# Kernel optimization log

Hardware: AMD Instinct MI355X
Metric: run time of the kernel (lower is better)

Reference implementation:

```python
import jax, jax.numpy as jnp
import numpy as np
from functools import partial

NODES = 50
IN_SZ = 12
HID = 6


def _conv(x, W, b):
    # x: [N, C, H, W], W: [O, I, 3, 3], pad 1 -> same H, W
    y = jax.lax.conv_general_dilated(x, W, window_strides=(1, 1),
                                     padding=((1, 1), (1, 1)),
                                     dimension_numbers=('NCHW', 'OIHW', 'NCHW'))
    return y + b[None, :, None, None]


def setup_inputs() -> dict:
    key = jax.random.key(0)
    ks = jax.random.split(key, 12)
    B, T = 4096, 12
    d = {}
    d['A_hat'] = jax.random.normal(ks[0], (NODES, NODES), dtype=jnp.float32)
    d['X'] = jax.random.normal(ks[1], (B, NODES, T, IN_SZ, 1), dtype=jnp.float32)
    s_ih = 1.0 / np.sqrt(HID)
    d['W_ih'] = jax.random.uniform(ks[2], (4 * HID, IN_SZ), jnp.float32, -s_ih, s_ih)
    d['W_hh'] = jax.random.uniform(ks[3], (4 * HID, HID), jnp.float32, -s_ih, s_ih)
    d['b_ih'] = jax.random.uniform(ks[4], (4 * HID,), jnp.float32, -s_ih, s_ih)
    d['b_hh'] = jax.random.uniform(ks[5], (4 * HID,), jnp.float32, -s_ih, s_ih)
    d['Wf1'] = jax.random.normal(ks[6], (100, 50, 3, 3), jnp.float32) * 0.05
    d['bf1'] = jnp.zeros((100,), jnp.float32)
    d['Wf2'] = jax.random.normal(ks[7], (100, 100, 3, 3), jnp.float32) * 0.05
    d['bf2'] = jnp.zeros((100,), jnp.float32)
    d['Wf3'] = jax.random.normal(ks[8], (50, 100, 3, 3), jnp.float32) * 0.05
    d['bf3'] = jnp.zeros((50,), jnp.float32)
    d['W_lean'] = jax.random.normal(ks[9], (HID, HID), jnp.float32) * 0.3
    d['b_lean'] = jnp.zeros((HID,), jnp.float32)
    return d


def reference(A_hat, X, W_ih, W_hh, b_ih, b_hh, Wf1, bf1, Wf2, bf2, Wf3, bf3, W_lean, b_lean):
    # out1: [S, 50, 12] with S = B*T; the Python loop over S becomes a scan
    out1 = jnp.squeeze(X, axis=4).reshape(-1, NODES, IN_SZ)

    def step(carry, x_t):
        h, c = carry  # each [50, 6]
        gates = x_t @ W_ih.T + b_ih + h @ W_hh.T + b_hh  # [50, 24]
        i, f, g, o = jnp.split(gates, 4, axis=-1)
        i = jax.nn.sigmoid(i)
        f = jax.nn.sigmoid(f)
        g = jnp.tanh(g)
        o = jax.nn.sigmoid(o)
        c_new = f * c + i * g
        h_new = o * jnp.tanh(c_new)
        h_new = jnp.tanh(h_new)  # module applies extra tanh and feeds it back
        return (h_new, c_new), h_new

    h0 = jnp.zeros((NODES, HID), dtype=X.dtype)
    c0 = jnp.zeros((NODES, HID), dtype=X.dtype)
    _, al = jax.lax.scan(step, (h0, c0), out1)  # al: [S, 50, 6]

    out2 = al.reshape(-1, NODES, HID, 1)  # [S, 50, 6, 1]
    f = jax.nn.relu(_conv(out2, Wf1, bf1))
    f = jax.nn.relu(_conv(f, Wf2, bf2))
    f = jax.nn.relu(_conv(f, Wf3, bf3))
    out = (f.reshape(-1, HID) @ W_lean.T + b_lean).reshape(-1, NODES, HID, 1)
    return out
```

## Files before the change

kernel.cpp:

```cpp
#include <hip/hip_runtime.h>

#define NCH 1536
#define CL 32
#define WM 16

typedef _Float16 half8 __attribute__((ext_vector_type(8)));
typedef float f32x4 __attribute__((ext_vector_type(4)));

#define ROWB 256
#define BUFB 17408
#define ALH_OFF 131072

__device__ __forceinline__ int swz(int srow, int b){ return srow*ROWB + (b ^ ((srow&7)<<4)); }

__device__ __forceinline__ unsigned short f2h_bits(float x){
  _Float16 h = (_Float16)x;
  return __builtin_bit_cast(unsigned short, h);
}

__device__ __forceinline__ float rcp_(float x){ return __builtin_amdgcn_rcpf(x); }
__device__ __forceinline__ float tanh_(float z){ return 1.f - 2.f*rcp_(1.f + __expf(2.f*z)); }

__global__ void pack_frags(const float* __restrict__ W1, const float* __restrict__ W2,
                           const float* __restrict__ W3, unsigned short* __restrict__ ws)
{
  int tid = blockIdx.x*256 + threadIdx.x;
  if (tid >= 174*512) return;
  int f = tid >> 9, e = tid & 511, l = e >> 3, j = e & 7;
  int d, ks, nt, I, O; const float* W;
  if (f < 42)      { int x = f;     int st = x/7;  nt = x%7; d = st/2; ks = st%2; I = 50;  O = 100; W = W1; }
  else if (f < 126){ int x = f-42;  int st = x/7;  nt = x%7; d = st/4; ks = st%4; I = 100; O = 100; W = W2; }
  else             { int x = f-126; int st = x/4;  nt = x%4; d = st/4; ks = st%4; I = 100; O = 50;  W = W3; }
  int k = ks*32 + ((l>>4)<<3) + j;
  int o = nt*16 + (l&15);
  float v = (k < I && o < O) ? W[((o*I + k)*3 + d)*3 + 1] : 0.f;
  ws[tid] = f2h_bits(v);
}

template<bool F16>
__global__ __launch_bounds__(128,2) void lstm_scan3(
    const float* __restrict__ X, const float* __restrict__ Wih,
    const float* __restrict__ Whh, const float* __restrict__ bih,
    const float* __restrict__ bhh, float* __restrict__ al32,
    unsigned short* __restrict__ al16)
{
  const int l = threadIdx.x & 63;
  const int wv = threadIdx.x >> 6;
  const int blk = blockIdx.x;
  const int p6 = blk/5, w = blk - p6*5;
  const int q = l/6, j = l - q*6;
  const bool active = (q < 10);
  const int n = w*10 + (active ? q : 0);
  const int sbase = active ? q*6 : 0;

  const int c0 = p6*6 + 3*wv;
  const int sAb = c0*CL, sBb = sAb + CL, sCb = sBb + CL;
  const int sALast = sAb + CL - 1, sBLast = sBb + CL - 1, sCLast = sCb + CL - 1;

  float wi[4][12], wh[4][6], bb[4];
  #pragma unroll
  for (int g=0; g<4; ++g){
    const int r = g*6 + j;
    const float4 w0 = *(const float4*)(Wih + r*12);
    const float4 w1 = *(const float4*)(Wih + r*12 + 4);
    const float4 w2 = *(const float4*)(Wih + r*12 + 8);
    wi[g][0]=w0.x; wi[g][1]=w0.y; wi[g][2]=w0.z; wi[g][3]=w0.w;
    wi[g][4]=w1.x; wi[g][5]=w1.y; wi[g][6]=w1.z; wi[g][7]=w1.w;
    wi[g][8]=w2.x; wi[g][9]=w2.y; wi[g][10]=w2.z; wi[g][11]=w2.w;
    const float2 h0 = *(const float2*)(Whh + r*6);
    const float2 h1 = *(const float2*)(Whh + r*6 + 2);
    const float2 h2 = *(const float2*)(Whh + r*6 + 4);
    wh[g][0]=h0.x; wh[g][1]=h0.y; wh[g][2]=h1.x;
    wh[g][3]=h1.y; wh[g][4]=h2.x; wh[g][5]=h2.y;
    bb[g] = bih[r] + bhh[r];
  }

  float hA[6], hB[6], hC[6], cA = 0.f, cB = 0.f, cC = 0.f;
  #pragma unroll
  for (int k=0;k<6;++k){ hA[k]=0.f; hB[k]=0.f; hC[k]=0.f; }

  const int sA0 = (c0==0) ? 0 : (sAb - WM);
  const int sB0 = sBb - WM;
  const int sC0 = sCb - WM;
  float4 xA0,xA1,xA2, xB0,xB1,xB2, xC0,xC1,xC2;
  { const float4* p = (const float4*)(X + (size_t)sA0*600 + n*12); xA0=p[0]; xA1=p[1]; xA2=p[2]; }
  { const float4* p = (const float4*)(X + (size_t)sB0*600 + n*12); xB0=p[0]; xB1=p[1]; xB2=p[2]; }
  { const float4* p = (const float4*)(X + (size_t)sC0*600 + n*12); xC0=p[0]; xC1=p[1]; xC2=p[2]; }

  auto step = [&](const float4& x0, const float4& x1, const float4& x2,
                  float* h, float& c) -> float {
    const float xr[12] = {x0.x,x0.y,x0.z,x0.w, x1.x,x1.y,x1.z,x1.w, x2.x,x2.y,x2.z,x2.w};
    float a0=bb[0], a1=bb[1], a2=bb[2], a3=bb[3];
    #pragma unroll
    for (int k=0;k<12;++k){ a0+=wi[0][k]*xr[k]; a1+=wi[1][k]*xr[k];
                            a2+=wi[2][k]*xr[k]; a3+=wi[3][k]*xr[k]; }
    #pragma unroll
    for (int k=0;k<6;++k){ a0+=wh[0][k]*h[k]; a1+=wh[1][k]*h[k];
                           a2+=wh[2][k]*h[k]; a3+=wh[3][k]*h[k]; }
    const float gi = rcp_(1.f + __expf(-a0));
    const float gf = rcp_(1.f + __expf(-a1));
    const float gg = 2.f*rcp_(1.f + __expf(-(a2+a2))) - 1.f;
    const float go = rcp_(1.f + __expf(-a3));
    c = gf*c + gi*gg;
    return tanh_(go * tanh_(c));
  };

  for (int i = -WM; i < CL; ++i){
    const int sA = sAb + i, sB = sBb + i, sC = sCb + i;
    const bool doA = (sA >= 0);

    float hnA = 0.f;
    if (doA){
      hnA = step(xA0,xA1,xA2, hA, cA);
      const int sn = (sA < sALast) ? sA+1 : sALast;
      const float4* xq = (const float4*)(X + (size_t)sn*600 + n*12);
      xA0 = xq[0]; xA1 = xq[1]; xA2 = xq[2];
    }
    float hnB;
    {
      hnB = step(xB0,xB1,xB2, hB, cB);
      const int sn = (sB < sBLast) ? sB+1 : sBLast;
      const float4* xq = (const float4*)(X + (size_t)sn*600 + n*12);
      xB0 = xq[0]; xB1 = xq[1]; xB2 = xq[2];
    }
    float hnC;
    {
      hnC = step(xC0,xC1,xC2, hC, cC);
      const int sn = (sC < sCLast) ? sC+1 : sCLast;
      const float4* xq = (const float4*)(X + (size_t)sn*600 + n*12);
      xC0 = xq[0]; xC1 = xq[1]; xC2 = xq[2];
    }

    if (active && i >= 0){
      const size_t oA = (size_t)sA*300 + n*6 + j;
      const size_t oB = (size_t)sB*300 + n*6 + j;
      const size_t oC = (size_t)sC*300 + n*6 + j;
      if (F16){ al16[oA] = f2h_bits(hnA); al16[oB] = f2h_bits(hnB); al16[oC] = f2h_bits(hnC); }
      else    { al32[oA] = hnA;           al32[oB] = hnB;           al32[oC] = hnC; }
    }
    #pragma unroll
    for (int k=0;k<6;++k){
      hA[k] = __shfl(hnA, sbase + k, 64);
      hB[k] = __shfl(hnB, sbase + k, 64);
      hC[k] = __shfl(hnC, sbase + k, 64);
    }
  }
}

template<int KS, int NTT, int NTG, bool LAST>
__device__ __forceinline__ void conv_layer2(
    char* lds, int inOff, int outOff, const unsigned short* __restrict__ wsU,
    int fbase, int ntOff, const float* __restrict__ bias, int O, int m0, int lane)
{
  f32x4 acc[2][NTG];
  #pragma unroll
  for (int m=0;m<2;m++)
    #pragma unroll
    for (int n=0;n<NTG;n++) acc[m][n] = (f32x4){0.f,0.f,0.f,0.f};

  const int ar = m0 + (lane & 15);
  const int abyte_g = (lane>>4)<<4;
  const int laneb = lane << 3;

  half8 a0c = *(const half8*)(lds + inOff + swz(ar, abyte_g));
  half8 a1c = *(const half8*)(lds + inOff + swz(ar + 16, abyte_g));
  half8 bc[NTG];
  {
    const unsigned short* p0 = wsU + (size_t)(fbase + ntOff)*512 + laneb;
    #pragma unroll
    for (int n=0;n<NTG;n++) bc[n] = *(const half8*)(p0 + n*512);
  }

  #pragma unroll
  for (int st=0; st<3*KS; ++st){
    half8 a0n, a1n, bn[NTG];
    if (st+1 < 3*KS){
      const int dn = (st+1)/KS, ksn = (st+1)%KS;
      a0n = *(const half8*)(lds + inOff + swz(ar + dn, ksn*64 + abyte_g));
      a1n = *(const half8*)(lds + inOff + swz(ar + 16 + dn, ksn*64 + abyte_g));
      const unsigned short* pn = wsU + (size_t)(fbase + (st+1)*NTT + ntOff)*512 + laneb;
      #pragma unroll
      for (int n=0;n<NTG;n++) bn[n] = *(const half8*)(pn + n*512);
    }
    #pragma unroll
    for (int n=0;n<NTG;n++){
      acc[0][n] = __builtin_amdgcn_mfma_f32_16x16x32_f16(a0c, bc[n], acc[0][n], 0, 0, 0);
      acc[1][n] = __builtin_amdgcn_mfma_f32_16x16x32_f16(a1c, bc[n], acc[1][n], 0, 0, 0);
    }
    if (st+1 < 3*KS){
      a0c = a0n; a1c = a1n;
      #pragma unroll
      for (int n=0;n<NTG;n++) bc[n] = bn[n];
    }
  }

  const int colBase = lane & 15;
  #pragma unroll
  for (int m=0;m<2;m++){
    const int rbase = m0 + m*16 + ((lane>>4)<<2);
    #pragma unroll
    for (int n=0;n<NTG;n++){
      const int col = (ntOff + n)*16 + colBase;
      if (col < O){
        const float b = bias[col];
        #pragma unroll
        for (int r=0;r<4;r++){
          const int crow = rbase + r;
          const int p8 = crow & 7;
          if (p8 >= 1 && p8 <= 6){
            const float v = fmaxf(acc[m][n][r] + b, 0.f);
            const int srow = crow + 1;
            if (LAST) *(float*)(lds + outOff + swz(srow, col*4)) = v;
            else      *(unsigned short*)(lds + outOff + swz(srow, col*2)) = f2h_bits(v);
          }
        }
      }
    }
  }
}

template<int KS, int NTT, int NTG>
__device__ __forceinline__ void conv_layer3_fused(
    char* lds, int inOff, const unsigned short* __restrict__ wsU,
    int fbase, int ntOff, const float* __restrict__ b3,
    const float* __restrict__ Wl, const float* __restrict__ bl,
    float* __restrict__ io, size_t base, int m0, int lane)
{
  f32x4 acc[2][NTG];
  #pragma unroll
  for (int m=0;m<2;m++)
    #pragma unroll
    for (int n=0;n<NTG;n++) acc[m][n] = (f32x4){0.f,0.f,0.f,0.f};

  const int ar = m0 + (lane & 15);
  const int abyte_g = (lane>>4)<<4;
  const int laneb = lane << 3;

  half8 a0c = *(const half8*)(lds + inOff + swz(ar, abyte_g));
  half8 a1c = *(const half8*)(lds + inOff + swz(ar + 16, abyte_g));
  half8 bc[NTG];
  {
    const unsigned short* p0 = wsU + (size_t)(fbase + ntOff)*512 + laneb;
    #pragma unroll
    for (int n=0;n<NTG;n++) bc[n] = *(const half8*)(p0 + n*512);
  }

  #pragma unroll
  for (int st=0; st<3*KS; ++st){
    half8 a0n, a1n, bn[NTG];
    if (st+1 < 3*KS){
      const int dn = (st+1)/KS, ksn = (st+1)%KS;
      a0n = *(const half8*)(lds + inOff + swz(ar + dn, ksn*64 + abyte_g));
      a1n = *(const half8*)(lds + inOff + swz(ar + 16 + dn, ksn*64 + abyte_g));
      const unsigned short* pn = wsU + (size_t)(fbase + (st+1)*NTT + ntOff)*512 + laneb;
      #pragma unroll
      for (int n=0;n<NTG;n++) bn[n] = *(const half8*)(pn + n*512);
    }
    #pragma unroll
    for (int n=0;n<NTG;n++){
      acc[0][n] = __builtin_amdgcn_mfma_f32_16x16x32_f16(a0c, bc[n], acc[0][n], 0, 0, 0);
      acc[1][n] = __builtin_amdgcn_mfma_f32_16x16x32_f16(a1c, bc[n], acc[1][n], 0, 0, 0);
    }
    if (st+1 < 3*KS){
      a0c = a0n; a1c = a1n;
      #pragma unroll
      for (int n=0;n<NTG;n++) bc[n] = bn[n];
    }
  }

  const int colBase = lane & 15;
  const int qg = lane >> 4;
  const bool hiHalf = (qg & 1);
  #pragma unroll
  for (int m=0;m<2;m++){
    const int sIdx = (m0 + m*16 + qg*4) >> 3;
    #pragma unroll
    for (int n=0;n<NTG;n++){
      const int col = (ntOff + n)*16 + colBase;
      const bool valid = (col < 50);
      const float b = valid ? b3[col] : 0.f;
      float vv[4];
      #pragma unroll
      for (int r=0;r<4;r++) vv[r] = fmaxf(acc[m][n][r] + b, 0.f);
      float tot[6];
      #pragma unroll
      for (int j=0;j<6;j++){
        float pj;
        if (!hiHalf) pj = Wl[j*6+0]*vv[1] + Wl[j*6+1]*vv[2] + Wl[j*6+2]*vv[3];
        else         pj = Wl[j*6+3]*vv[0] + Wl[j*6+4]*vv[1] + Wl[j*6+5]*vv[2];
        tot[j] = pj + __shfl_xor(pj, 16, 64);
      }
      if (valid && !hiHalf){
        float* dst = io + base + (size_t)sIdx*300 + col*6;
        float2 p0 = {tot[0]+bl[0], tot[1]+bl[1]};
        float2 p1 = {tot[2]+bl[2], tot[3]+bl[3]};
        float2 p2 = {tot[4]+bl[4], tot[5]+bl[5]};
        *(float2*)(dst+0) = p0;
        *(float2*)(dst+2) = p1;
        *(float2*)(dst+4) = p2;
      }
    }
  }
}

template<bool ALH>
__global__ __launch_bounds__(256,4) void conv_mfma_kernel(
    float* __restrict__ io, const unsigned short* __restrict__ alh,
    const unsigned short* __restrict__ wsU,
    const float* __restrict__ b1, const float* __restrict__ b2, const float* __restrict__ b3,
    const float* __restrict__ Wl, const float* __restrict__ bl)
{
  __shared__ __align__(16) char lds[2*BUFB];
  const int t = threadIdx.x;
  const int lane = t & 63, w = t >> 6;
  const int mg = w >> 1, ng = w & 1;
  const int m0 = mg*32;
  const size_t base = (size_t)blockIdx.x * 2400;

  for (int i = t; i < (2*BUFB)/16; i += 256) ((f32x4*)lds)[i] = (f32x4){0.f,0.f,0.f,0.f};
  __syncthreads();

  if (ALH){
    const unsigned short* ap = alh + base;
    for (int idx = t; idx < 400; idx += 256){
      const int s = idx/50, n = idx - (idx/50)*50;
      const unsigned short* pp = ap + s*300 + n*6;
      const int r0 = s*8 + 2;
      #pragma unroll
      for (int y=0; y<6; ++y)
        *(unsigned short*)(lds + swz(r0 + y, n*2)) = pp[y];
    }
  } else {
    for (int idx = t; idx < 2400; idx += 256){
      const float v = io[base + idx];
      const int s = idx/300, rr = idx%300;
      const int ch = rr/6, y = rr%6;
      *(unsigned short*)(lds + swz(s*8 + y + 2, ch*2)) = f2h_bits(v);
    }
  }
  __syncthreads();

  if (ng == 0) conv_layer2<2,7,4,false>(lds, 0,    BUFB, wsU, 0,   0, b1, 100, m0, lane);
  else         conv_layer2<2,7,3,false>(lds, 0,    BUFB, wsU, 0,   4, b1, 100, m0, lane);
  __syncthreads();
  if (ng == 0) conv_layer2<4,7,4,false>(lds, BUFB, 0,    wsU, 42,  0, b2, 100, m0, lane);
  else         conv_layer2<4,7,3,false>(lds, BUFB, 0,    wsU, 42,  4, b2, 100, m0, lane);
  __syncthreads();
  if (ng == 0) conv_layer3_fused<4,4,2>(lds, 0, wsU, 126, 0, b3, Wl, bl, io, base, m0, lane);
  else         conv_layer3_fused<4,4,2>(lds, 0, wsU, 126, 2, b3, Wl, bl, io, base, m0, lane);
}

__device__ __forceinline__ float wraw(const float* __restrict__ W, int I, int i, int d, int o){
  return W[((o*I + i)*3 + d)*3 + 1];
}
template<int NS>
__device__ void conv_layer_valu(const float (* __restrict__ in)[100][8],
                                float (* __restrict__ outb)[100][8],
                                int I, const float* __restrict__ W,
                                const float* __restrict__ bias, int o, int s0)
{
  float acc[NS][6];
  const float b = bias[o];
  #pragma unroll
  for (int s=0;s<NS;s++)
    #pragma unroll
    for (int y=0;y<6;y++) acc[s][y]=b;
  for (int i=0;i<I;i++){
    const float w0 = wraw(W,I,i,0,o), w1 = wraw(W,I,i,1,o), w2 = wraw(W,I,i,2,o);
    #pragma unroll
    for (int s=0;s<NS;s++){
      const float4 r0 = *(const float4*)&in[s0+s][i][0];
      const float4 r1 = *(const float4*)&in[s0+s][i][4];
      acc[s][0] += w1*r0.x + w2*r0.y;
      acc[s][1] += w0*r0.x + w1*r0.y + w2*r0.z;
      acc[s][2] += w0*r0.y + w1*r0.z + w2*r0.w;
      acc[s][3] += w0*r0.z + w1*r0.w + w2*r1.x;
      acc[s][4] += w0*r0.w + w1*r1.x + w2*r1.y;
      acc[s][5] += w0*r1.x + w1*r1.y;
    }
  }
  #pragma unroll
  for (int s=0;s<NS;s++){
    float4 v0; float2 v1;
    v0.x = fmaxf(acc[s][0],0.f); v0.y = fmaxf(acc[s][1],0.f);
    v0.z = fmaxf(acc[s][2],0.f); v0.w = fmaxf(acc[s][3],0.f);
    v1.x = fmaxf(acc[s][4],0.f); v1.y = fmaxf(acc[s][5],0.f);
    *(float4*)&outb[s0+s][o][0] = v0;
    *(float2*)&outb[s0+s][o][4] = v1;
  }
}
__global__ __launch_bounds__(256,1) void conv_kernel_fb(
    float* __restrict__ io,
    const float* __restrict__ W1, const float* __restrict__ b1,
    const float* __restrict__ W2, const float* __restrict__ b2,
    const float* __restrict__ W3, const float* __restrict__ b3,
    const float* __restrict__ Wl, const float* __restrict__ bl)
{
  __shared__ float A[8][100][8];
  __shared__ float B[8][100][8];
  const int t = threadIdx.x;
  const size_t base = (size_t)blockIdx.x * 2400;
  for (int idx=t; idx<800; idx+=256){
    const int s = idx/100, ch = idx%100;
    A[s][ch][6]=0.f; A[s][ch][7]=0.f; B[s][ch][6]=0.f; B[s][ch][7]=0.f;
  }
  for (int idx=t; idx<2400; idx+=256){
    const float v = io[base + idx];
    const int s = idx/300, rr = idx%300;
    A[s][rr/6][rr%6] = v;
  }
  __syncthreads();
  const int w = t>>6, lane = t&63;
  { const int sh = w>>1, o = (w&1)*50 + lane;
    if (lane < 50) conv_layer_valu<4>(A, B, 50, W1, b1, o, sh*4); }
  __syncthreads();
  { const int sh = w>>1, o = (w&1)*50 + lane;
    if (lane < 50) conv_layer_valu<4>(B, A, 100, W2, b2, o, sh*4); }
  __syncthreads();
  { if (lane < 50) conv_layer_valu<2>(A, B, 100, W3, b3, lane, w*2); }
  __syncthreads();
  for (int idx=t; idx<2400; idx+=256){
    const int s = idx/300, rr = idx%300, n = rr/6, j = rr%6;
    const float4 r0 = *(const float4*)&B[s][n][0];
    const float2 r1 = *(const float2*)&B[s][n][4];
    io[base + idx] = bl[j] + Wl[j*6+0]*r0.x + Wl[j*6+1]*r0.y + Wl[j*6+2]*r0.z
                   + Wl[j*6+3]*r0.w + Wl[j*6+4]*r1.x + Wl[j*6+5]*r1.y;
  }
}

extern "C" void kernel_launch(void* const* d_in, const int* in_sizes, int n_in,
                              void* d_out, int out_size, void* d_ws, size_t ws_size,
                              hipStream_t stream)
{
  const float* X    = (const float*)d_in[1];
  const float* Wih  = (const float*)d_in[2];
  const float* Whh  = (const float*)d_in[3];
  const float* bih  = (const float*)d_in[4];
  const float* bhh  = (const float*)d_in[5];
  const float* Wf1  = (const float*)d_in[6];
  const float* bf1  = (const float*)d_in[7];
  const float* Wf2  = (const float*)d_in[8];
  const float* bf2  = (const float*)d_in[9];
  const float* Wf3  = (const float*)d_in[10];
  const float* bf3  = (const float*)d_in[11];
  const float* Wl   = (const float*)d_in[12];
  const float* bl   = (const float*)d_in[13];
  float* out = (float*)d_out;
  unsigned short* wsU = (unsigned short*)d_ws;

  const bool packed = (ws_size >= 174*512*sizeof(unsigned short));
  const bool bigws  = (ws_size >= (size_t)(ALH_OFF + 49152ull*300ull)*2ull);

  if (packed)
    hipLaunchKernelGGL(pack_frags, dim3(348), dim3(256), 0, stream,
                       Wf1, Wf2, Wf3, wsU);

  if (bigws && packed){
    unsigned short* alh = wsU + ALH_OFF;
    hipLaunchKernelGGL((lstm_scan3<true>), dim3((NCH/6)*5), dim3(128), 0, stream,
                       X, Wih, Whh, bih, bhh, nullptr, alh);
    hipLaunchKernelGGL((conv_mfma_kernel<true>), dim3(6144), dim3(256), 0, stream,
                       out, alh, wsU, bf1, bf2, bf3, Wl, bl);
  } else {
    hipLaunchKernelGGL((lstm_scan3<false>), dim3((NCH/6)*5), dim3(128), 0, stream,
                       X, Wih, Whh, bih, bhh, out, nullptr);
    if (packed)
      hipLaunchKernelGGL((conv_mfma_kernel<false>), dim3(6144), dim3(256), 0, stream,
                         out, nullptr, wsU, bf1, bf2, bf3, Wl, bl);
    else
      hipLaunchKernelGGL(conv_kernel_fb, dim3(6144), dim3(256), 0, stream,
                         out, Wf1, bf1, Wf2, bf2, Wf3, bf3, Wl, bl);
  }
}
```

Before: 216.3 us.

## Make each wave own two samples in conv chain, removing block barriers

Replaces the block-cooperative conv kernel on the workspace path with a per-wave kernel. Each wave loads two samples (16 padded rows) into its own private pair of LDS buffers and runs all three conv layers plus the lean projection alone, so no __syncthreads are needed. Each wave now computes all output tiles for one 16-row M tile instead of two M tiles over part of N, which raises weight-fragment reads per MFMA. LDS use drops to 36 KB per block. The explicit software prefetch of next-step A/B fragments is also removed in favour of plain loads, leaving scheduling to the compiler.

```diff
diff --git a/kernel.cpp b/kernel.cpp
--- a/kernel.cpp
+++ b/kernel.cpp
@@ -9,6 +9,7 @@
 
 #define ROWB 256
 #define BUFB 17408
+#define WREG 4608
 #define ALH_OFF 131072
 
 __device__ __forceinline__ int swz(int srow, int b){ return srow*ROWB + (b ^ ((srow&7)<<4)); }
@@ -147,6 +148,131 @@
   }
 }
 
+__device__ __forceinline__ int swzL(int r, int b){ return r*ROWB + (b ^ ((r&7)<<4)); }
+
+template<int KS, int NTT>
+__device__ __forceinline__ void wave_layer(
+    const char* __restrict__ inR, char* __restrict__ outR,
+    const unsigned short* __restrict__ wsU, int fbase,
+    const float* __restrict__ bias, int O, int lane)
+{
+  f32x4 acc[NTT];
+  #pragma unroll
+  for (int n=0;n<NTT;n++) acc[n] = (f32x4){0.f,0.f,0.f,0.f};
+  const int arl = lane & 15;
+  const int ag = (lane>>4)<<4;
+  const int laneb = lane << 3;
+  #pragma unroll
+  for (int st=0; st<3*KS; ++st){
+    const int d = st/KS, ks = st%KS;
+    const half8 a = *(const half8*)(inR + swzL(arl + d, ks*64 + ag));
+    const unsigned short* pf = wsU + (size_t)(fbase + st*NTT)*512 + laneb;
+    #pragma unroll
+    for (int n=0;n<NTT;n++){
+      const half8 b = *(const half8*)(pf + n*512);
+      acc[n] = __builtin_amdgcn_mfma_f32_16x16x32_f16(a, b, acc[n], 0, 0, 0);
+    }
+  }
+  const int colBase = lane & 15;
+  const int mBase = (lane>>4)<<2;
+  #pragma unroll
+  for (int n=0;n<NTT;n++){
+    const int col = n*16 + colBase;
+    if (col < O){
+      const float b = bias[col];
+      #pragma unroll
+      for (int r=0;r<4;r++){
+        const int ro = mBase + r + 1;
+        if ((ro & 7) >= 2)
+          *(unsigned short*)(outR + swzL(ro, col*2)) = f2h_bits(fmaxf(acc[n][r] + b, 0.f));
+      }
+    }
+  }
+}
+
+template<int KS, int NTT>
+__device__ __forceinline__ void wave_l3_lean(
+    const char* __restrict__ inR, const unsigned short* __restrict__ wsU, int fbase,
+    const float* __restrict__ b3, const float* __restrict__ Wl, const float* __restrict__ bl,
+    float* __restrict__ io, int gs0, int lane)
+{
+  f32x4 acc[NTT];
+  #pragma unroll
+  for (int n=0;n<NTT;n++) acc[n] = (f32x4){0.f,0.f,0.f,0.f};
+  const int arl = lane & 15;
+  const int ag = (lane>>4)<<4;
+  const int laneb = lane << 3;
+  #pragma unroll
+  for (int st=0; st<3*KS; ++st){
+    const int d = st/KS, ks = st%KS;
+    const half8 a = *(const half8*)(inR + swzL(arl + d, ks*64 + ag));
+    const unsigned short* pf = wsU + (size_t)(fbase + st*NTT)*512 + laneb;
+    #pragma unroll
+    for (int n=0;n<NTT;n++){
+      const half8 b = *(const half8*)(pf + n*512);
+      acc[n] = __builtin_amdgcn_mfma_f32_16x16x32_f16(a, b, acc[n], 0, 0, 0);
+    }
+  }
+  const int colBase = lane & 15;
+  const int qg = lane >> 4;
+  const bool hiHalf = (qg & 1);
+  const int sIdx = gs0 + (qg >> 1);
+  #pragma unroll
+  for (int n=0;n<NTT;n++){
+    const int col = n*16 + colBase;
+    const bool valid = (col < 50);
+    const float b = valid ? b3[col] : 0.f;
+    float vv[4];
+    #pragma unroll
+    for (int r=0;r<4;r++) vv[r] = fmaxf(acc[n][r] + b, 0.f);
+    float tot[6];
+    #pragma unroll
+    for (int j=0;j<6;j++){
+      float pj;
+      if (!hiHalf) pj = Wl[j*6+0]*vv[1] + Wl[j*6+1]*vv[2] + Wl[j*6+2]*vv[3];
+      else         pj = Wl[j*6+3]*vv[0] + Wl[j*6+4]*vv[1] + Wl[j*6+5]*vv[2];
+      tot[j] = pj + __shfl_xor(pj, 16, 64);
+    }
+    if (valid && !hiHalf){
+      float* dst = io + (size_t)sIdx*300 + col*6;
+      float2 p0 = {tot[0]+bl[0], tot[1]+bl[1]};
+      float2 p1 = {tot[2]+bl[2], tot[3]+bl[3]};
+      float2 p2 = {tot[4]+bl[4], tot[5]+bl[5]};
+      *(float2*)(dst+0) = p0;
+      *(float2*)(dst+2) = p1;
+      *(float2*)(dst+4) = p2;
+    }
+  }
+}
+
+__global__ __launch_bounds__(256,4) void conv_wave_kernel(
+    float* __restrict__ io, const unsigned short* __restrict__ alh,
+    const unsigned short* __restrict__ wsU,
+    const float* __restrict__ b1, const float* __restrict__ b2, const float* __restrict__ b3,
+    const float* __restrict__ Wl, const float* __restrict__ bl)
+{
+  __shared__ __align__(16) char lds[4*2*WREG];
+  const int t = threadIdx.x, lane = t & 63, wv = t >> 6;
+  char* R0 = lds + wv*(2*WREG);
+  char* R1 = R0 + WREG;
+  const int gs0 = blockIdx.x*8 + 2*wv;
+
+  for (int i = lane; i < (2*WREG)/16; i += 64)
+    *(f32x4*)(R0 + i*16) = (f32x4){0.f,0.f,0.f,0.f};
+
+  {
+    const unsigned short* ap = alh + (size_t)gs0*300;
+    for (int idx = lane; idx < 600; idx += 64){
+      const int sl = idx/300, rr = idx - sl*300;
+      const int n = rr/6, y = rr - n*6;
+      *(unsigned short*)(R0 + swzL(sl*8 + 2 + y, n*2)) = ap[idx];
+    }
+  }
+  wave_layer<2,7>(R0, R1, wsU, 0,   b1, 100, lane);
+  wave_layer<4,7>(R1, R0, wsU, 42,  b2, 100, lane);
+  wave_l3_lean<4,4>(R0, wsU, 126, b3, Wl, bl, io, gs0, lane);
+}
+
 template<int KS, int NTT, int NTG, bool LAST>
 __device__ __forceinline__ void conv_layer2(
     char* lds, int inOff, int outOff, const unsigned short* __restrict__ wsU,
@@ -157,43 +283,22 @@
   for (int m=0;m<2;m++)
     #pragma unroll
     for (int n=0;n<NTG;n++) acc[m][n] = (f32x4){0.f,0.f,0.f,0.f};
-
   const int ar = m0 + (lane & 15);
   const int abyte_g = (lane>>4)<<4;
   const int laneb = lane << 3;
-
-  half8 a0c = *(const half8*)(lds + inOff + swz(ar, abyte_g));
-  half8 a1c = *(const half8*)(lds + inOff + swz(ar + 16, abyte_g));
-  half8 bc[NTG];
-  {
-    const unsigned short* p0 = wsU + (size_t)(fbase + ntOff)*512 + laneb;
-    #pragma unroll
-    for (int n=0;n<NTG;n++) bc[n] = *(const half8*)(p0 + n*512);
-  }
-
   #pragma unroll
   for (int st=0; st<3*KS; ++st){
-    half8 a0n, a1n, bn[NTG];
-    if (st+1 < 3*KS){
-      const int dn = (st+1)/KS, ksn = (st+1)%KS;
-      a0n = *(const half8*)(lds + inOff + swz(ar + dn, ksn*64 + abyte_g));
-      a1n = *(const half8*)(lds + inOff + swz(ar + 16 + dn, ksn*64 + abyte_g));
-      const unsigned short* pn = wsU + (size_t)(fbase + (st+1)*NTT + ntOff)*512 + laneb;
-      #pragma unroll
-      for (int n=0;n<NTG;n++) bn[n] = *(const half8*)(pn + n*512);
-    }
+    const int d = st/KS, ks = st%KS;
+    const half8 a0 = *(const half8*)(lds + inOff + swz(ar + d, ks*64 + abyte_g));
+    const half8 a1 = *(const half8*)(lds + inOff + swz(ar + 16 + d, ks*64 + abyte_g));
+    const unsigned short* pf = wsU + (size_t)(fbase + st*NTT + ntOff)*512 + laneb;
     #pragma unroll
     for (int n=0;n<NTG;n++){
-      acc[0][n] = __builtin_amdgcn_mfma_f32_16x16x32_f16(a0c, bc[n], acc[0][n], 0, 0, 0);
-      acc[1][n] = __builtin_amdgcn_mfma_f32_16x16x32_f16(a1c, bc[n], acc[1][n], 0, 0, 0);
-    }
-    if (st+1 < 3*KS){
-      a0c = a0n; a1c = a1n;
-      #pragma unroll
-      for (int n=0;n<NTG;n++) bc[n] = bn[n];
-    }
-  }
-
+      const half8 b = *(const half8*)(pf + n*512);
+      acc[0][n] = __builtin_amdgcn_mfma_f32_16x16x32_f16(a0, b, acc[0][n], 0, 0, 0);
+      acc[1][n] = __builtin_amdgcn_mfma_f32_16x16x32_f16(a1, b, acc[1][n], 0, 0, 0);
+    }
+  }
   const int colBase = lane & 15;
   #pragma unroll
   for (int m=0;m<2;m++){
@@ -219,94 +324,8 @@
   }
 }
 
-template<int KS, int NTT, int NTG>
-__device__ __forceinline__ void conv_layer3_fused(
-    char* lds, int inOff, const unsigned short* __restrict__ wsU,
-    int fbase, int ntOff, const float* __restrict__ b3,
-    const float* __restrict__ Wl, const float* __restrict__ bl,
-    float* __restrict__ io, size_t base, int m0, int lane)
-{
-  f32x4 acc[2][NTG];
-  #pragma unroll
-  for (int m=0;m<2;m++)
-    #pragma unroll
-    for (int n=0;n<NTG;n++) acc[m][n] = (f32x4){0.f,0.f,0.f,0.f};
-
-  const int ar = m0 + (lane & 15);
-  const int abyte_g = (lane>>4)<<4;
-  const int laneb = lane << 3;
-
-  half8 a0c = *(const half8*)(lds + inOff + swz(ar, abyte_g));
-  half8 a1c = *(const half8*)(lds + inOff + swz(ar + 16, abyte_g));
-  half8 bc[NTG];
-  {
-    const unsigned short* p0 = wsU + (size_t)(fbase + ntOff)*512 + laneb;
-    #pragma unroll
-    for (int n=0;n<NTG;n++) bc[n] = *(const half8*)(p0 + n*512);
-  }
-
-  #pragma unroll
-  for (int st=0; st<3*KS; ++st){
-    half8 a0n, a1n, bn[NTG];
-    if (st+1 < 3*KS){
-      const int dn = (st+1)/KS, ksn = (st+1)%KS;
-      a0n = *(const half8*)(lds + inOff + swz(ar + dn, ksn*64 + abyte_g));
-      a1n = *(const half8*)(lds + inOff + swz(ar + 16 + dn, ksn*64 + abyte_g));
-      const unsigned short* pn = wsU + (size_t)(fbase + (st+1)*NTT + ntOff)*512 + laneb;
-      #pragma unroll
-      for (int n=0;n<NTG;n++) bn[n] = *(const half8*)(pn + n*512);
-    }
-    #pragma unroll
-    for (int n=0;n<NTG;n++){
-      acc[0][n] = __builtin_amdgcn_mfma_f32_16x16x32_f16(a0c, bc[n], acc[0][n], 0, 0, 0);
-      acc[1][n] = __builtin_amdgcn_mfma_f32_16x16x32_f16(a1c, bc[n], acc[1][n], 0, 0, 0);
-    }
-    if (st+1 < 3*KS){
-      a0c = a0n; a1c = a1n;
-      #pragma unroll
-      for (int n=0;n<NTG;n++) bc[n] = bn[n];
-    }
-  }
-
-  const int colBase = lane & 15;
-  const int qg = lane >> 4;
-  const bool hiHalf = (qg & 1);
-  #pragma unroll
-  for (int m=0;m<2;m++){
-    const int sIdx = (m0 + m*16 + qg*4) >> 3;
-    #pragma unroll
-    for (int n=0;n<NTG;n++){
-      const int col = (ntOff + n)*16 + colBase;
-      const bool valid = (col < 50);
-      const float b = valid ? b3[col] : 0.f;
-      float vv[4];
-      #pragma unroll
-      for (int r=0;r<4;r++) vv[r] = fmaxf(acc[m][n][r] + b, 0.f);
-      float tot[6];
-      #pragma unroll
-      for (int j=0;j<6;j++){
-        float pj;
-        if (!hiHalf) pj = Wl[j*6+0]*vv[1] + Wl[j*6+1]*vv[2] + Wl[j*6+2]*vv[3];
-        else         pj = Wl[j*6+3]*vv[0] + Wl[j*6+4]*vv[1] + Wl[j*6+5]*vv[2];
-        tot[j] = pj + __shfl_xor(pj, 16, 64);
-      }
-      if (valid && !hiHalf){
-        float* dst = io + base + (size_t)sIdx*300 + col*6;
-        float2 p0 = {tot[0]+bl[0], tot[1]+bl[1]};
-        float2 p1 = {tot[2]+bl[2], tot[3]+bl[3]};
-        float2 p2 = {tot[4]+bl[4], tot[5]+bl[5]};
-        *(float2*)(dst+0) = p0;
-        *(float2*)(dst+2) = p1;
-        *(float2*)(dst+4) = p2;
-      }
-    }
-  }
-}
-
-template<bool ALH>
-__global__ __launch_bounds__(256,4) void conv_mfma_kernel(
-    float* __restrict__ io, const unsigned short* __restrict__ alh,
-    const unsigned short* __restrict__ wsU,
+__global__ __launch_bounds__(256,4) void conv_mfma_f32in(
+    float* __restrict__ io, const unsigned short* __restrict__ wsU,
     const float* __restrict__ b1, const float* __restrict__ b2, const float* __restrict__ b3,
     const float* __restrict__ Wl, const float* __restrict__ bl)
 {
@@ -319,35 +338,71 @@
 
   for (int i = t; i < (2*BUFB)/16; i += 256) ((f32x4*)lds)[i] = (f32x4){0.f,0.f,0.f,0.f};
   __syncthreads();
-
-  if (ALH){
-    const unsigned short* ap = alh + base;
-    for (int idx = t; idx < 400; idx += 256){
-      const int s = idx/50, n = idx - (idx/50)*50;
-      const unsigned short* pp = ap + s*300 + n*6;
-      const int r0 = s*8 + 2;
-      #pragma unroll
-      for (int y=0; y<6; ++y)
-        *(unsigned short*)(lds + swz(r0 + y, n*2)) = pp[y];
-    }
-  } else {
-    for (int idx = t; idx < 2400; idx += 256){
-      const float v = io[base + idx];
-      const int s = idx/300, rr = idx%300;
-      const int ch = rr/6, y = rr%6;
-      *(unsigned short*)(lds + swz(s*8 + y + 2, ch*2)) = f2h_bits(v);
-    }
-  }
-  __syncthreads();
-
+  for (int idx = t; idx < 2400; idx += 256){
+    const float v = io[base + idx];
+    const int s = idx/300, rr = idx%300;
+    const int ch = rr/6, y = rr%6;
+    *(unsigned short*)(lds + swz(s*8 + y + 2, ch*2)) = f2h_bits(v);
+  }
+  __syncthreads();
   if (ng == 0) conv_layer2<2,7,4,false>(lds, 0,    BUFB, wsU, 0,   0, b1, 100, m0, lane);
   else         conv_layer2<2,7,3,false>(lds, 0,    BUFB, wsU, 0,   4, b1, 100, m0, lane);
   __syncthreads();
   if (ng == 0) conv_layer2<4,7,4,false>(lds, BUFB, 0,    wsU, 42,  0, b2, 100, m0, lane);
   else         conv_layer2<4,7,3,false>(lds, BUFB, 0,    wsU, 42,  4, b2, 100, m0, lane);
   __syncthreads();
-  if (ng == 0) conv_layer3_fused<4,4,2>(lds, 0, wsU, 126, 0, b3, Wl, bl, io, base, m0, lane);
-  else         conv_layer3_fused<4,4,2>(lds, 0, wsU, 126, 2, b3, Wl, bl, io, base, m0, lane);
+  {
+    f32x4 acc[2][2];
+    #pragma unroll
+    for (int m=0;m<2;m++){ acc[m][0]=(f32x4){0,0,0,0}; acc[m][1]=(f32x4){0,0,0,0}; }
+    const int ntOff = ng ? 2 : 0;
+    const int ar = m0 + (lane & 15);
+    const int abyte_g = (lane>>4)<<4;
+    const int laneb = lane << 3;
+    #pragma unroll
+    for (int st=0; st<12; ++st){
+      const int d = st/4, ks = st%4;
+      const half8 a0 = *(const half8*)(lds + swz(ar + d, ks*64 + abyte_g));
+      const half8 a1 = *(const half8*)(lds + swz(ar + 16 + d, ks*64 + abyte_g));
+      const unsigned short* pf = wsU + (size_t)(126 + st*4 + ntOff)*512 + laneb;
+      #pragma unroll
+      for (int n=0;n<2;n++){
+        const half8 b = *(const half8*)(pf + n*512);
+        acc[0][n] = __builtin_amdgcn_mfma_f32_16x16x32_f16(a0, b, acc[0][n], 0, 0, 0);
+        acc[1][n] = __builtin_amdgcn_mfma_f32_16x16x32_f16(a1, b, acc[1][n], 0, 0, 0);
+      }
+    }
+    const int colBase = lane & 15;
+    const int qg = lane >> 4;
+    const bool hiHalf = (qg & 1);
+    #pragma unroll
+    for (int m=0;m<2;m++){
+      const int sIdx = (m0 + m*16 + qg*4) >> 3;
+      #pragma unroll
+      for (int n=0;n<2;n++){
+        const int col = (ntOff + n)*16 + colBase;
+        const bool valid = (col < 50);
+        const float b = valid ? b3[col] : 0.f;
+        float vv[4];
+        #pragma unroll
+        for (int r=0;r<4;r++) vv[r] = fmaxf(acc[m][n][r] + b, 0.f);
+        float tot[6];
+        #pragma unroll
+        for (int j=0;j<6;j++){
+          float pj;
+          if (!hiHalf) pj = Wl[j*6+0]*vv[1] + Wl[j*6+1]*vv[2] + Wl[j*6+2]*vv[3];
+          else         pj = Wl[j*6+3]*vv[0] + Wl[j*6+4]*vv[1] + Wl[j*6+5]*vv[2];
+          tot[j] = pj + __shfl_xor(pj, 16, 64);
+        }
+        if (valid && !hiHalf){
+          float* dst = io + base + (size_t)sIdx*300 + col*6;
+          *(float2*)(dst+0) = (float2){tot[0]+bl[0], tot[1]+bl[1]};
+          *(float2*)(dst+2) = (float2){tot[2]+bl[2], tot[3]+bl[3]};
+          *(float2*)(dst+4) = (float2){tot[4]+bl[4], tot[5]+bl[5]};
+        }
+      }
+    }
+  }
 }
 
 __device__ __forceinline__ float wraw(const float* __restrict__ W, int I, int i, int d, int o){
@@ -459,14 +514,14 @@
     unsigned short* alh = wsU + ALH_OFF;
     hipLaunchKernelGGL((lstm_scan3<true>), dim3((NCH/6)*5), dim3(128), 0, stream,
                        X, Wih, Whh, bih, bhh, nullptr, alh);
-    hipLaunchKernelGGL((conv_mfma_kernel<true>), dim3(6144), dim3(256), 0, stream,
+    hipLaunchKernelGGL(conv_wave_kernel, dim3(6144), dim3(256), 0, stream,
                        out, alh, wsU, bf1, bf2, bf3, Wl, bl);
   } else {
     hipLaunchKernelGGL((lstm_scan3<false>), dim3((NCH/6)*5), dim3(128), 0, stream,
                        X, Wih, Whh, bih, bhh, out, nullptr);
     if (packed)
-      hipLaunchKernelGGL((conv_mfma_kernel<false>), dim3(6144), dim3(256), 0, stream,
-                         out, nullptr, wsU, bf1, bf2, bf3, Wl, bl);
+      hipLaunchKernelGGL(conv_mfma_f32in, dim3(6144), dim3(256), 0, stream,
+                         out, wsU, bf1, bf2, bf3, Wl, bl);
     else
       hipLaunchKernelGGL(conv_kernel_fb, dim3(6144), dim3(256), 0, stream,
                          out, Wf1, bf1, Wf2, bf2, Wf3, bf3, Wl, bl);
```

Result: slower. 287.3 us (+32.8%).
